# Performance work log

Measured on AMD Instinct MI355X. Metric: run time of the kernel, lower is better.

The kernel has to match this reference:

```python
import jax, jax.numpy as jnp
import numpy as np

B, C, H, W = 4, 256, 64, 64
E = C // 8  # embedding_channels = inChannels // k


def setup_inputs() -> dict:
    key = jax.random.key(0)
    ks = jax.random.split(key, 9)
    sc = 1.0 / np.sqrt(C)
    so = 1.0 / np.sqrt(E)
    return {
        "x": jax.random.normal(ks[0], (B, C, H, W), dtype=jnp.float32),
        "Wk": jax.random.normal(ks[1], (E, C), dtype=jnp.float32) * sc,
        "bk": jax.random.normal(ks[2], (E,), dtype=jnp.float32) * 0.01,
        "Wq": jax.random.normal(ks[3], (E, C), dtype=jnp.float32) * sc,
        "bq": jax.random.normal(ks[4], (E,), dtype=jnp.float32) * 0.01,
        "Wv": jax.random.normal(ks[5], (E, C), dtype=jnp.float32) * sc,
        "bv": jax.random.normal(ks[6], (E,), dtype=jnp.float32) * 0.01,
        "Wo": jax.random.normal(ks[7], (C, E), dtype=jnp.float32) * so,
        "bo": jax.random.normal(ks[8], (C,), dtype=jnp.float32) * 0.01,
    }


def reference(x, Wk, bk, Wq, bq, Wv, bv, Wo, bo):
    b, c, h, w = x.shape
    n = h * w
    gamma = jnp.float32(0.5)  # non-learned branch (learned=False default)

    def conv1x1(inp, Wt, bt):
        # 1x1 conv == channel-mixing matmul: [b,c,h,w] x [e,c] -> [b,e,h,w]
        return jnp.einsum('bchw,ec->behw', inp, Wt) + bt[None, :, None, None]

    f = conv1x1(x, Wk, bk).reshape(b, -1, n)  # key   [b,E,N]
    g = conv1x1(x, Wq, bq).reshape(b, -1, n)  # query [b,E,N]
    hx = conv1x1(x, Wv, bv).reshape(b, -1, n)  # value [b,E,N]

    s = jnp.einsum('bei,bej->bij', f, g)       # f^T @ g, [b,N,N]
    beta = jax.nn.softmax(s, axis=1)           # softmax over dim 1 (rows) as in torch
    v = jnp.einsum('bei,bij->bej', hx, beta)   # h @ beta, [b,E,N]
    v = v.reshape(b, -1, h, w)

    o = jnp.einsum('behw,ce->bchw', v, Wo) + bo[None, :, None, None]
    y = gamma * o + x
    return y, o, gamma
```

## Files before the change

kernel.cpp:

```cpp
#include <hip/hip_runtime.h>

#define B_ 4
#define C_ 256
#define N_ 4096
#define E_ 32

typedef _Float16 f16x8 __attribute__((ext_vector_type(8)));
typedef _Float16 f16x4 __attribute__((ext_vector_type(4)));
typedef _Float16 f16x2 __attribute__((ext_vector_type(2)));
typedef float f32x4 __attribute__((ext_vector_type(4)));

#define LOG2E 1.44269504088896f
#define EXP2(x) __builtin_amdgcn_exp2f(x)
#define PKRTZ(a, b) __builtin_bit_cast(f16x2, __builtin_amdgcn_cvt_pkrtz((a), (b)))

#define XSWZ(row, col) ((col) ^ ((((row) >> 2) & 7) << 3))

__global__ __launch_bounds__(256) void proj_kernel(
    const float* __restrict__ x,
    const float* __restrict__ Wk, const float* __restrict__ bk,
    const float* __restrict__ Wq, const float* __restrict__ bq,
    const float* __restrict__ Wv, const float* __restrict__ bv,
    const float* __restrict__ Wo,
    _Float16* __restrict__ Qb, _Float16* __restrict__ Kb, _Float16* __restrict__ Vt,
    _Float16* __restrict__ Wof16, float* __restrict__ out)
{
    const int b  = blockIdx.x >> 7;
    const int n0 = (blockIdx.x & 127) << 5;
    const int t    = threadIdx.x;
    const int lane = t & 63;
    const int wave = t >> 6;
    const int l15  = lane & 15;
    const int quad = lane >> 4;

    if (blockIdx.x < 256 && t < 8) {
        float4 wv = ((const float4*)(Wo + blockIdx.x * E_))[t];
        f16x4 tp = {(_Float16)wv.x, (_Float16)wv.y, (_Float16)wv.z, (_Float16)wv.w};
        *(f16x4*)&Wof16[blockIdx.x * E_ + t * 4] = tp;
    }
    if (blockIdx.x == 0 && t == 0)
        out[(size_t)2 * B_ * C_ * N_] = 0.5f;

    __shared__ _Float16 xT[32][264];
    __shared__ _Float16 Wl[32][264];
    __shared__ _Float16 vT[32][44];

    for (int i4 = t; i4 < (32 * 256) / 4; i4 += 256) {
        int j4 = (i4 & 7) * 4;
        int c  = i4 >> 3;
        float4 xv = *(const float4*)(x + (size_t)(b * C_ + c) * N_ + n0 + j4);
        xT[j4 + 0][XSWZ(j4 + 0, c)] = (_Float16)xv.x;
        xT[j4 + 1][XSWZ(j4 + 1, c)] = (_Float16)xv.y;
        xT[j4 + 2][XSWZ(j4 + 2, c)] = (_Float16)xv.z;
        xT[j4 + 3][XSWZ(j4 + 3, c)] = (_Float16)xv.w;
    }

    const float* Ws[3] = {Wk, Wq, Wv};
    const float* bs[3] = {bk, bq, bv};

    const int rowg = wave >> 1;
    const int et   = wave & 1;
    const int row  = rowg * 16 + l15;
    f16x8 Bf[8];

    for (int m = 0; m < 3; ++m) {
        for (int i4 = t; i4 < (E_ * C_) / 4; i4 += 256) {
            float4 wv = ((const float4*)Ws[m])[i4];
            int e = (i4 * 4) >> 8, c = (i4 * 4) & 255;
            f16x4 tp = {(_Float16)wv.x, (_Float16)wv.y, (_Float16)wv.z, (_Float16)wv.w};
            *(f16x4*)&Wl[e][XSWZ(e, c)] = tp;
        }
        __syncthreads();
        if (m == 0) {
            #pragma unroll
            for (int kk = 0; kk < 8; ++kk)
                Bf[kk] = *(const f16x8*)&xT[row][XSWZ(row, kk * 32 + quad * 8)];
        }
        const float sc = (m == 1) ? LOG2E : 1.0f;
        const float* bias = bs[m];
        f32x4 acc = {0.f, 0.f, 0.f, 0.f};
        #pragma unroll
        for (int kk = 0; kk < 8; ++kk) {
            const int e = et * 16 + l15;
            f16x8 Af = *(const f16x8*)&Wl[e][XSWZ(e, kk * 32 + quad * 8)];
            acc = __builtin_amdgcn_mfma_f32_16x16x32_f16(Af, Bf[kk], acc, 0, 0, 0);
        }
        const int n  = n0 + row;
        const int e0 = et * 16 + quad * 4;
        if (m == 2) {
            #pragma unroll
            for (int r = 0; r < 4; ++r)
                vT[e0 + r][row] = (_Float16)(acc[r] + bias[e0 + r]);
        } else {
            f16x4 st;
            #pragma unroll
            for (int r = 0; r < 4; ++r)
                st[r] = (_Float16)((acc[r] + bias[e0 + r]) * sc);
            _Float16* dst = (m == 0) ? Kb : Qb;
            *(f16x4*)&dst[(size_t)(b * N_ + n) * E_ + e0] = st;
        }
        __syncthreads();
    }

    if (t < 128) {
        const int e_s = t >> 2;
        const int nb  = t & 3;
        f16x8 v = *(const f16x8*)&vT[e_s][nb * 8];
        size_t base = ((size_t)(b * 128 + (n0 >> 5)) * 32 + e_s) * 32 + nb * 8;
        *(f16x8*)&Vt[base] = v;
    }
}

__global__ __launch_bounds__(512, 4) void attn_kernel(
    const _Float16* __restrict__ Qb, const _Float16* __restrict__ Kb,
    const _Float16* __restrict__ Vt, const _Float16* __restrict__ Wof16,
    const float* __restrict__ bo, const float* __restrict__ x,
    float* __restrict__ out)
{
    const int wave = threadIdx.x >> 6;
    const int lane = threadIdx.x & 63;
    const int l15  = lane & 15, quad = lane >> 4;
    const int jg   = blockIdx.x;
    const int b    = jg >> 7;
    const int j0   = (jg & 127) << 5;

    __shared__ __align__(16) char big[8][2][2176];
    __shared__ float    mls[8][2][2][16];
    __shared__ _Float16 Om[2][16][40];

    f16x8 Qf[2];
    #pragma unroll
    for (int cc = 0; cc < 2; ++cc)
        Qf[cc] = *(const f16x8*)(Qb + (size_t)(b * N_ + j0 + cc * 16 + l15) * E_ + quad * 8);

    f32x4 O0c[2], O1c[2];
    float mrow[2], lsum[2];
    #pragma unroll
    for (int cc = 0; cc < 2; ++cc) {
        O0c[cc] = (f32x4){0, 0, 0, 0}; O1c[cc] = (f32x4){0, 0, 0, 0};
        mrow[cc] = -1e30f; lsum[cc] = 0.f;
    }

    const _Float16* Kp = Kb + (size_t)b * N_ * E_ + (size_t)(wave << 9) * E_;
    const _Float16* Vp = Vt + ((size_t)(b * 128 + wave * 16) << 10);

    f16x8 K0 = *(const f16x8*)(Kp + (size_t)l15 * E_ + quad * 8);
    f16x8 K1 = *(const f16x8*)(Kp + (size_t)(16 + l15) * E_ + quad * 8);
    f16x8 Va = *(const f16x8*)(Vp + l15 * 32 + quad * 8);
    f16x8 Vc = *(const f16x8*)(Vp + (16 + l15) * 32 + quad * 8);

    #pragma unroll 2
    for (int it = 0; it < 16; ++it) {
        const int i0n = (it + 1) << 5;
        f32x4 S0[2], S1[2];
        f32x4 z = {0, 0, 0, 0};
        __builtin_amdgcn_s_setprio(1);
        #pragma unroll
        for (int cc = 0; cc < 2; ++cc) {
            S0[cc] = __builtin_amdgcn_mfma_f32_16x16x32_f16(K0, Qf[cc], z, 0, 0, 0);
            S1[cc] = __builtin_amdgcn_mfma_f32_16x16x32_f16(K1, Qf[cc], z, 0, 0, 0);
        }
        __builtin_amdgcn_s_setprio(0);
        K0 = *(const f16x8*)(Kp + (size_t)(i0n + l15) * E_ + quad * 8);
        K1 = *(const f16x8*)(Kp + (size_t)(i0n + 16 + l15) * E_ + quad * 8);

        #pragma unroll
        for (int cc = 0; cc < 2; ++cc) {
            float mxa = fmaxf(fmaxf(S0[cc][0], S0[cc][1]), S0[cc][2]);
            float mxb = fmaxf(fmaxf(S0[cc][3], S1[cc][0]), S1[cc][1]);
            float mxc = fmaxf(fmaxf(S1[cc][2], S1[cc][3]), mxa);
            float mxl = fmaxf(mxb, mxc);
            if (__any(mxl > mrow[cc] + 8.f)) {
                float mx = fmaxf(mxl, __shfl_xor(mxl, 16));
                mx = fmaxf(mx, __shfl_xor(mx, 32));
                float mnew  = fmaxf(mrow[cc], mx);
                float alpha = EXP2(mrow[cc] - mnew);
                mrow[cc] = mnew;
                lsum[cc] *= alpha;
                O0c[cc] *= alpha;
                O1c[cc] *= alpha;
            }
            float m0 = mrow[cc];
            float p00 = EXP2(S0[cc][0] - m0), p01 = EXP2(S0[cc][1] - m0);
            float p02 = EXP2(S0[cc][2] - m0), p03 = EXP2(S0[cc][3] - m0);
            float p10 = EXP2(S1[cc][0] - m0), p11 = EXP2(S1[cc][1] - m0);
            float p12 = EXP2(S1[cc][2] - m0), p13 = EXP2(S1[cc][3] - m0);
            lsum[cc] += ((p00 + p01) + (p02 + p03)) + ((p10 + p11) + (p12 + p13));

            f16x2 a0 = PKRTZ(p00, p01);
            f16x2 a1 = PKRTZ(p02, p03);
            f16x2 a2 = PKRTZ(p10, p11);
            f16x2 a3 = PKRTZ(p12, p13);
            f16x4 w0 = {a0[0], a0[1], a1[0], a1[1]};
            f16x4 w1 = {a2[0], a2[1], a3[0], a3[1]};
            _Float16 (*pb)[40] = (_Float16 (*)[40])(big[wave][cc]);
            *(f16x4*)&pb[l15][quad * 4]      = w0;
            *(f16x4*)&pb[l15][16 + quad * 4] = w1;
        }
        f16x8 P0, P1;
        {
            _Float16 (*pb0)[40] = (_Float16 (*)[40])(big[wave][0]);
            _Float16 (*pb1)[40] = (_Float16 (*)[40])(big[wave][1]);
            P0 = *(const f16x8*)&pb0[l15][quad * 8];
            P1 = *(const f16x8*)&pb1[l15][quad * 8];
        }
        __builtin_amdgcn_s_setprio(1);
        O0c[0] = __builtin_amdgcn_mfma_f32_16x16x32_f16(Va, P0, O0c[0], 0, 0, 0);
        O1c[0] = __builtin_amdgcn_mfma_f32_16x16x32_f16(Vc, P0, O1c[0], 0, 0, 0);
        O0c[1] = __builtin_amdgcn_mfma_f32_16x16x32_f16(Va, P1, O0c[1], 0, 0, 0);
        O1c[1] = __builtin_amdgcn_mfma_f32_16x16x32_f16(Vc, P1, O1c[1], 0, 0, 0);
        __builtin_amdgcn_s_setprio(0);
        Va = *(const f16x8*)(Vp + (i0n << 5) + l15 * 32 + quad * 8);
        Vc = *(const f16x8*)(Vp + (i0n << 5) + (16 + l15) * 32 + quad * 8);
    }

    #pragma unroll
    for (int cc = 0; cc < 2; ++cc) {
        float ls = lsum[cc];
        ls += __shfl_xor(ls, 16);
        ls += __shfl_xor(ls, 32);
        if (quad == 0) { mls[wave][0][cc][l15] = mrow[cc]; mls[wave][1][cc][l15] = ls; }
    }
    __syncthreads();

    #pragma unroll
    for (int cc = 0; cc < 2; ++cc) {
        float M = -1e30f, ms[8], ls[8];
        #pragma unroll
        for (int s = 0; s < 8; ++s) {
            ms[s] = mls[s][0][cc][l15]; ls[s] = mls[s][1][cc][l15];
            M = fmaxf(M, ms[s]);
        }
        float L = 0.f;
        #pragma unroll
        for (int s = 0; s < 8; ++s) L += ls[s] * EXP2(ms[s] - M);
        const float w = EXP2(mrow[cc] - M) / L;
        float (*osum)[34] = (float (*)[34])(big[wave][cc]);
        *(f32x4*)&osum[l15][quad * 4]      = O0c[cc] * w;
        *(f32x4*)&osum[l15][16 + quad * 4] = O1c[cc] * w;
    }
    __syncthreads();

    {
        const int j = threadIdx.x >> 5;
        const int e = threadIdx.x & 31;
        #pragma unroll
        for (int cc = 0; cc < 2; ++cc) {
            float a = 0.f;
            #pragma unroll
            for (int s = 0; s < 8; ++s)
                a += ((const float (*)[34])(big[s][cc]))[j][e];
            Om[cc][j][e] = (_Float16)a;
        }
    }
    __syncthreads();

    f16x8 Bf2[2];
    #pragma unroll
    for (int cc = 0; cc < 2; ++cc)
        Bf2[cc] = *(const f16x8*)&Om[cc][l15][quad * 8];
    float* out_y = out + (size_t)b * C_ * N_;
    float* out_o = out + (size_t)B_ * C_ * N_ + (size_t)b * C_ * N_;
    const float* xb = x + (size_t)b * C_ * N_;
    #pragma unroll
    for (int ct = 0; ct < 2; ++ct) {
        const int c0 = wave * 32 + ct * 16;
        f16x8 Af = *(const f16x8*)(Wof16 + (size_t)(c0 + l15) * E_ + quad * 8);
        f32x4 acc[2];
        f32x4 z = {0, 0, 0, 0};
        #pragma unroll
        for (int cc = 0; cc < 2; ++cc)
            acc[cc] = __builtin_amdgcn_mfma_f32_16x16x32_f16(Af, Bf2[cc], z, 0, 0, 0);
        #pragma unroll
        for (int r = 0; r < 4; ++r) {
            const int c = c0 + quad * 4 + r;
            #pragma unroll
            for (int cc = 0; cc < 2; ++cc) {
                size_t idx = (size_t)c * N_ + j0 + cc * 16 + l15;
                float ov = acc[cc][r] + bo[c];
                out_o[idx] = ov;
                out_y[idx] = 0.5f * ov + xb[idx];
            }
        }
    }
}

extern "C" void kernel_launch(void* const* d_in, const int* in_sizes, int n_in,
                              void* d_out, int out_size, void* d_ws, size_t ws_size,
                              hipStream_t stream)
{
    const float* x  = (const float*)d_in[0];
    const float* Wk = (const float*)d_in[1];
    const float* bk = (const float*)d_in[2];
    const float* Wq = (const float*)d_in[3];
    const float* bq = (const float*)d_in[4];
    const float* Wv = (const float*)d_in[5];
    const float* bv = (const float*)d_in[6];
    const float* Wo = (const float*)d_in[7];
    const float* bo = (const float*)d_in[8];
    float* out = (float*)d_out;

    char* ws = (char*)d_ws;
    _Float16* Qb    = (_Float16*)(ws);
    _Float16* Kb    = (_Float16*)(ws + (1u << 20));
    _Float16* Vt    = (_Float16*)(ws + (2u << 20));
    _Float16* Wof16 = (_Float16*)(ws + (3u << 20));

    proj_kernel<<<dim3(512), dim3(256), 0, stream>>>(
        x, Wk, bk, Wq, bq, Wv, bv, Wo, Qb, Kb, Vt, Wof16, out);
    attn_kernel<<<dim3(B_ * (N_ / 32)), dim3(512), 0, stream>>>(
        Qb, Kb, Vt, Wof16, bo, x, out);
}
```

Measured before the change: 122.8 us.

## Process 64 keys per attention iteration and fold max subtraction into MFMA accumulator

The attention loop now handles 64 keys per iteration instead of 32. It issues eight score MFMAs and eight PV MFMAs per step and prefetches four K and four V fragments ahead, which halves the trip count, gives more independent work per iteration, and drops the unroll-2 pragma. The running row max is kept as a negated offset that seeds the score MFMA accumulators. This removes the per-element subtraction before exp2, and on a rescale the scores are adjusted in place. In exchange, register pressure and the LDS staging buffer grow, which may affect occupancy under the 512-thread, 4-block launch bound.

```diff
diff --git a/kernel.cpp b/kernel.cpp
--- a/kernel.cpp
+++ b/kernel.cpp
@@ -124,7 +124,7 @@
     const int b    = jg >> 7;
     const int j0   = (jg & 127) << 5;
 
-    __shared__ __align__(16) char big[8][2][2176];
+    __shared__ __align__(16) char big[8][2][2304];
     __shared__ float    mls[8][2][2][16];
     __shared__ _Float16 Om[2][16][40];
 
@@ -134,84 +134,119 @@
         Qf[cc] = *(const f16x8*)(Qb + (size_t)(b * N_ + j0 + cc * 16 + l15) * E_ + quad * 8);
 
     f32x4 O0c[2], O1c[2];
-    float mrow[2], lsum[2];
+    float mneg[2], lsum[2];
     #pragma unroll
     for (int cc = 0; cc < 2; ++cc) {
         O0c[cc] = (f32x4){0, 0, 0, 0}; O1c[cc] = (f32x4){0, 0, 0, 0};
-        mrow[cc] = -1e30f; lsum[cc] = 0.f;
+        mneg[cc] = 0.f; lsum[cc] = 0.f;
     }
 
     const _Float16* Kp = Kb + (size_t)b * N_ * E_ + (size_t)(wave << 9) * E_;
     const _Float16* Vp = Vt + ((size_t)(b * 128 + wave * 16) << 10);
 
-    f16x8 K0 = *(const f16x8*)(Kp + (size_t)l15 * E_ + quad * 8);
+    f16x8 K0 = *(const f16x8*)(Kp + (size_t)(l15) * E_ + quad * 8);
     f16x8 K1 = *(const f16x8*)(Kp + (size_t)(16 + l15) * E_ + quad * 8);
-    f16x8 Va = *(const f16x8*)(Vp + l15 * 32 + quad * 8);
-    f16x8 Vc = *(const f16x8*)(Vp + (16 + l15) * 32 + quad * 8);
-
-    #pragma unroll 2
-    for (int it = 0; it < 16; ++it) {
-        const int i0n = (it + 1) << 5;
-        f32x4 S0[2], S1[2];
-        f32x4 z = {0, 0, 0, 0};
-        __builtin_amdgcn_s_setprio(1);
-        #pragma unroll
-        for (int cc = 0; cc < 2; ++cc) {
-            S0[cc] = __builtin_amdgcn_mfma_f32_16x16x32_f16(K0, Qf[cc], z, 0, 0, 0);
-            S1[cc] = __builtin_amdgcn_mfma_f32_16x16x32_f16(K1, Qf[cc], z, 0, 0, 0);
-        }
-        __builtin_amdgcn_s_setprio(0);
+    f16x8 K2 = *(const f16x8*)(Kp + (size_t)(32 + l15) * E_ + quad * 8);
+    f16x8 K3 = *(const f16x8*)(Kp + (size_t)(48 + l15) * E_ + quad * 8);
+    f16x8 Va0 = *(const f16x8*)(Vp + l15 * 32 + quad * 8);
+    f16x8 Vc0 = *(const f16x8*)(Vp + (16 + l15) * 32 + quad * 8);
+    f16x8 Va1 = *(const f16x8*)(Vp + 1024 + l15 * 32 + quad * 8);
+    f16x8 Vc1 = *(const f16x8*)(Vp + 1024 + (16 + l15) * 32 + quad * 8);
+
+    for (int it = 0; it < 8; ++it) {
+        const int i0n = (it + 1) << 6;
+        f32x4 S[2][4];
+        {
+            f32x4 c0 = {mneg[0], mneg[0], mneg[0], mneg[0]};
+            f32x4 c1 = {mneg[1], mneg[1], mneg[1], mneg[1]};
+            __builtin_amdgcn_s_setprio(1);
+            S[0][0] = __builtin_amdgcn_mfma_f32_16x16x32_f16(K0, Qf[0], c0, 0, 0, 0);
+            S[0][1] = __builtin_amdgcn_mfma_f32_16x16x32_f16(K1, Qf[0], c0, 0, 0, 0);
+            S[0][2] = __builtin_amdgcn_mfma_f32_16x16x32_f16(K2, Qf[0], c0, 0, 0, 0);
+            S[0][3] = __builtin_amdgcn_mfma_f32_16x16x32_f16(K3, Qf[0], c0, 0, 0, 0);
+            S[1][0] = __builtin_amdgcn_mfma_f32_16x16x32_f16(K0, Qf[1], c1, 0, 0, 0);
+            S[1][1] = __builtin_amdgcn_mfma_f32_16x16x32_f16(K1, Qf[1], c1, 0, 0, 0);
+            S[1][2] = __builtin_amdgcn_mfma_f32_16x16x32_f16(K2, Qf[1], c1, 0, 0, 0);
+            S[1][3] = __builtin_amdgcn_mfma_f32_16x16x32_f16(K3, Qf[1], c1, 0, 0, 0);
+            __builtin_amdgcn_s_setprio(0);
+        }
         K0 = *(const f16x8*)(Kp + (size_t)(i0n + l15) * E_ + quad * 8);
         K1 = *(const f16x8*)(Kp + (size_t)(i0n + 16 + l15) * E_ + quad * 8);
+        K2 = *(const f16x8*)(Kp + (size_t)(i0n + 32 + l15) * E_ + quad * 8);
+        K3 = *(const f16x8*)(Kp + (size_t)(i0n + 48 + l15) * E_ + quad * 8);
 
         #pragma unroll
         for (int cc = 0; cc < 2; ++cc) {
-            float mxa = fmaxf(fmaxf(S0[cc][0], S0[cc][1]), S0[cc][2]);
-            float mxb = fmaxf(fmaxf(S0[cc][3], S1[cc][0]), S1[cc][1]);
-            float mxc = fmaxf(fmaxf(S1[cc][2], S1[cc][3]), mxa);
-            float mxl = fmaxf(mxb, mxc);
-            if (__any(mxl > mrow[cc] + 8.f)) {
+            float t0 = fmaxf(fmaxf(S[cc][0][0], S[cc][0][1]), S[cc][0][2]);
+            float t1 = fmaxf(fmaxf(S[cc][0][3], S[cc][1][0]), S[cc][1][1]);
+            float t2 = fmaxf(fmaxf(S[cc][1][2], S[cc][1][3]), S[cc][2][0]);
+            float t3 = fmaxf(fmaxf(S[cc][2][1], S[cc][2][2]), S[cc][2][3]);
+            float t4 = fmaxf(fmaxf(S[cc][3][0], S[cc][3][1]), S[cc][3][2]);
+            float mxl = fmaxf(fmaxf(fmaxf(t0, t1), t2),
+                              fmaxf(fmaxf(t3, t4), S[cc][3][3]));
+            if (__any(mxl > 8.f)) {
                 float mx = fmaxf(mxl, __shfl_xor(mxl, 16));
                 mx = fmaxf(mx, __shfl_xor(mx, 32));
-                float mnew  = fmaxf(mrow[cc], mx);
-                float alpha = EXP2(mrow[cc] - mnew);
-                mrow[cc] = mnew;
+                float mc = fmaxf(mx, 0.f);
+                float alpha = EXP2(-mc);
+                mneg[cc] -= mc;
                 lsum[cc] *= alpha;
                 O0c[cc] *= alpha;
                 O1c[cc] *= alpha;
+                #pragma unroll
+                for (int kt = 0; kt < 4; ++kt)
+                    #pragma unroll
+                    for (int r = 0; r < 4; ++r)
+                        S[cc][kt][r] -= mc;
             }
-            float m0 = mrow[cc];
-            float p00 = EXP2(S0[cc][0] - m0), p01 = EXP2(S0[cc][1] - m0);
-            float p02 = EXP2(S0[cc][2] - m0), p03 = EXP2(S0[cc][3] - m0);
-            float p10 = EXP2(S1[cc][0] - m0), p11 = EXP2(S1[cc][1] - m0);
-            float p12 = EXP2(S1[cc][2] - m0), p13 = EXP2(S1[cc][3] - m0);
-            lsum[cc] += ((p00 + p01) + (p02 + p03)) + ((p10 + p11) + (p12 + p13));
-
-            f16x2 a0 = PKRTZ(p00, p01);
-            f16x2 a1 = PKRTZ(p02, p03);
-            f16x2 a2 = PKRTZ(p10, p11);
-            f16x2 a3 = PKRTZ(p12, p13);
-            f16x4 w0 = {a0[0], a0[1], a1[0], a1[1]};
-            f16x4 w1 = {a2[0], a2[1], a3[0], a3[1]};
-            _Float16 (*pb)[40] = (_Float16 (*)[40])(big[wave][cc]);
-            *(f16x4*)&pb[l15][quad * 4]      = w0;
-            *(f16x4*)&pb[l15][16 + quad * 4] = w1;
-        }
-        f16x8 P0, P1;
+            float p0  = EXP2(S[cc][0][0]), p1  = EXP2(S[cc][0][1]);
+            float p2  = EXP2(S[cc][0][2]), p3  = EXP2(S[cc][0][3]);
+            float p4  = EXP2(S[cc][1][0]), p5  = EXP2(S[cc][1][1]);
+            float p6  = EXP2(S[cc][1][2]), p7  = EXP2(S[cc][1][3]);
+            float p8  = EXP2(S[cc][2][0]), p9  = EXP2(S[cc][2][1]);
+            float p10 = EXP2(S[cc][2][2]), p11 = EXP2(S[cc][2][3]);
+            float p12 = EXP2(S[cc][3][0]), p13 = EXP2(S[cc][3][1]);
+            float p14 = EXP2(S[cc][3][2]), p15 = EXP2(S[cc][3][3]);
+            lsum[cc] += (((p0 + p1) + (p2 + p3)) + ((p4 + p5) + (p6 + p7)))
+                      + (((p8 + p9) + (p10 + p11)) + ((p12 + p13) + (p14 + p15)));
+
+            f16x2 a0 = PKRTZ(p0,  p1),  a1 = PKRTZ(p2,  p3);
+            f16x2 a2 = PKRTZ(p4,  p5),  a3 = PKRTZ(p6,  p7);
+            f16x2 a4 = PKRTZ(p8,  p9),  a5 = PKRTZ(p10, p11);
+            f16x2 a6 = PKRTZ(p12, p13), a7 = PKRTZ(p14, p15);
+            f16x4 wA0 = {a0[0], a0[1], a1[0], a1[1]};
+            f16x4 wA1 = {a2[0], a2[1], a3[0], a3[1]};
+            f16x4 wB0 = {a4[0], a4[1], a5[0], a5[1]};
+            f16x4 wB1 = {a6[0], a6[1], a7[0], a7[1]};
+            _Float16 (*pb)[72] = (_Float16 (*)[72])(big[wave][cc]);
+            *(f16x4*)&pb[l15][quad * 4]      = wA0;
+            *(f16x4*)&pb[l15][16 + quad * 4] = wA1;
+            *(f16x4*)&pb[l15][32 + quad * 4] = wB0;
+            *(f16x4*)&pb[l15][48 + quad * 4] = wB1;
+        }
+        f16x8 PA0, PB0, PA1, PB1;
         {
-            _Float16 (*pb0)[40] = (_Float16 (*)[40])(big[wave][0]);
-            _Float16 (*pb1)[40] = (_Float16 (*)[40])(big[wave][1]);
-            P0 = *(const f16x8*)&pb0[l15][quad * 8];
-            P1 = *(const f16x8*)&pb1[l15][quad * 8];
+            _Float16 (*pb0)[72] = (_Float16 (*)[72])(big[wave][0]);
+            _Float16 (*pb1)[72] = (_Float16 (*)[72])(big[wave][1]);
+            PA0 = *(const f16x8*)&pb0[l15][quad * 8];
+            PB0 = *(const f16x8*)&pb0[l15][32 + quad * 8];
+            PA1 = *(const f16x8*)&pb1[l15][quad * 8];
+            PB1 = *(const f16x8*)&pb1[l15][32 + quad * 8];
         }
         __builtin_amdgcn_s_setprio(1);
-        O0c[0] = __builtin_amdgcn_mfma_f32_16x16x32_f16(Va, P0, O0c[0], 0, 0, 0);
-        O1c[0] = __builtin_amdgcn_mfma_f32_16x16x32_f16(Vc, P0, O1c[0], 0, 0, 0);
-        O0c[1] = __builtin_amdgcn_mfma_f32_16x16x32_f16(Va, P1, O0c[1], 0, 0, 0);
-        O1c[1] = __builtin_amdgcn_mfma_f32_16x16x32_f16(Vc, P1, O1c[1], 0, 0, 0);
+        O0c[0] = __builtin_amdgcn_mfma_f32_16x16x32_f16(Va0, PA0, O0c[0], 0, 0, 0);
+        O1c[0] = __builtin_amdgcn_mfma_f32_16x16x32_f16(Vc0, PA0, O1c[0], 0, 0, 0);
+        O0c[1] = __builtin_amdgcn_mfma_f32_16x16x32_f16(Va0, PA1, O0c[1], 0, 0, 0);
+        O1c[1] = __builtin_amdgcn_mfma_f32_16x16x32_f16(Vc0, PA1, O1c[1], 0, 0, 0);
+        O0c[0] = __builtin_amdgcn_mfma_f32_16x16x32_f16(Va1, PB0, O0c[0], 0, 0, 0);
+        O1c[0] = __builtin_amdgcn_mfma_f32_16x16x32_f16(Vc1, PB0, O1c[0], 0, 0, 0);
+        O0c[1] = __builtin_amdgcn_mfma_f32_16x16x32_f16(Va1, PB1, O0c[1], 0, 0, 0);
+        O1c[1] = __builtin_amdgcn_mfma_f32_16x16x32_f16(Vc1, PB1, O1c[1], 0, 0, 0);
         __builtin_amdgcn_s_setprio(0);
-        Va = *(const f16x8*)(Vp + (i0n << 5) + l15 * 32 + quad * 8);
-        Vc = *(const f16x8*)(Vp + (i0n << 5) + (16 + l15) * 32 + quad * 8);
+        Va0 = *(const f16x8*)(Vp + (i0n << 5) + l15 * 32 + quad * 8);
+        Vc0 = *(const f16x8*)(Vp + (i0n << 5) + (16 + l15) * 32 + quad * 8);
+        Va1 = *(const f16x8*)(Vp + (i0n << 5) + 1024 + l15 * 32 + quad * 8);
+        Vc1 = *(const f16x8*)(Vp + (i0n << 5) + 1024 + (16 + l15) * 32 + quad * 8);
     }
 
     #pragma unroll
@@ -219,7 +254,7 @@
         float ls = lsum[cc];
         ls += __shfl_xor(ls, 16);
         ls += __shfl_xor(ls, 32);
-        if (quad == 0) { mls[wave][0][cc][l15] = mrow[cc]; mls[wave][1][cc][l15] = ls; }
+        if (quad == 0) { mls[wave][0][cc][l15] = -mneg[cc]; mls[wave][1][cc][l15] = ls; }
     }
     __syncthreads();
 
@@ -234,7 +269,7 @@
         float L = 0.f;
         #pragma unroll
         for (int s = 0; s < 8; ++s) L += ls[s] * EXP2(ms[s] - M);
-        const float w = EXP2(mrow[cc] - M) / L;
+        const float w = EXP2(-mneg[cc] - M) / L;
         float (*osum)[34] = (float (*)[34])(big[wave][cc]);
         *(f32x4*)&osum[l15][quad * 4]      = O0c[cc] * w;
         *(f32x4*)&osum[l15][16 + quad * 4] = O1c[cc] * w;
```

Measured after the change: 121.2 us (median of 2 runs). Within noise of the previous version (-1.3%).
